# Kernel tuning notes

Hardware: AMD Instinct MI355X
Metric: run time of the kernel (lower is better)

Reference implementation:

```python
import jax, jax.numpy as jnp
import numpy as np

IN_F, HID, OUT_F, N_HEADS, BATCH = 256, 512, 2048, 8, 4096


def _kaiming_uniform(key, shape, fan_in):
    # kaiming_uniform_ with a=sqrt(5): gain = sqrt(2/(1+5)) = 1/sqrt(3)
    gain = 1.0 / np.sqrt(3.0)
    bound = gain * np.sqrt(3.0 / fan_in)  # = sqrt(1/fan_in)
    return jax.random.uniform(key, shape, jnp.float32, -bound, bound)


def setup_inputs() -> dict:
    key = jax.random.key(0)
    kx, ki, k1, k2, k3, k4 = jax.random.split(key, 6)
    X = jax.random.normal(kx, (BATCH, IN_F), jnp.float32)
    X_head_idx = jax.random.randint(ki, (BATCH,), 0, N_HEADS)
    # layer 1: in -> hidden
    W1 = _kaiming_uniform(k1, (N_HEADS, IN_F, HID), IN_F)
    b1 = jax.random.uniform(k2, (N_HEADS, HID), jnp.float32,
                            -1.0 / np.sqrt(IN_F), 1.0 / np.sqrt(IN_F))
    # layer 2: hidden -> out
    W2 = _kaiming_uniform(k3, (N_HEADS, HID, OUT_F), HID)
    b2 = jax.random.uniform(k4, (N_HEADS, OUT_F), jnp.float32,
                            -1.0 / np.sqrt(HID), 1.0 / np.sqrt(HID))
    return {"X": X, "X_head_idx": X_head_idx, "W1": W1, "b1": b1,
            "W2": W2, "b2": b2}


def _selective_linear(x, idx, W, b):
    # x: [B, in], W: [H, in, out], b: [H, out], idx: [B]
    # compute all heads densely, then select each sample's head
    y = jnp.einsum('bi,hio->bho', x, W) + b[None]   # [B, H, out]
    return jnp.take_along_axis(y, idx[:, None, None], axis=1)[:, 0, :]


def reference(X, X_head_idx, W1, b1, W2, b2):
    h = _selective_linear(X, X_head_idx, W1, b1)
    h = jax.nn.relu(h)
    out = _selective_linear(h, X_head_idx, W2, b2)
    return out
```

## Files before the change

### kernel.cpp

```cpp
#include <hip/hip_runtime.h>

#define IN_F 256
#define HID 512
#define OUT_F 2048
#define N_HEADS 8
#define BATCH 4096

typedef __bf16 bf16_t;
typedef bf16_t bf16x8 __attribute__((ext_vector_type(8)));
typedef float f32x4 __attribute__((ext_vector_type(4)));

typedef __attribute__((address_space(1))) const unsigned int gu32;
typedef __attribute__((address_space(3))) unsigned int lu32;

__device__ inline unsigned short f2bf(float f) {
  union { float f; unsigned u; } v; v.f = f;
  unsigned u = v.u;
  unsigned r = (u + 0x7FFFu + ((u >> 16) & 1u)) >> 16;
  return (unsigned short)r;
}

__global__ __launch_bounds__(1024) void bucket_kernel(const int* __restrict__ idx,
                                                      int* __restrict__ order,
                                                      int* __restrict__ offsets) {
  __shared__ int cnt[N_HEADS];
  __shared__ int base[N_HEADS + 1];
  __shared__ int cur[N_HEADS];
  int tid = threadIdx.x;
  if (tid < N_HEADS) cnt[tid] = 0;
  __syncthreads();
  for (int i = tid; i < BATCH; i += 1024) atomicAdd(&cnt[idx[i]], 1);
  __syncthreads();
  if (tid == 0) {
    int acc = 0;
    for (int h = 0; h < N_HEADS; ++h) { base[h] = acc; cur[h] = acc; acc += cnt[h]; }
    base[N_HEADS] = acc;
  }
  __syncthreads();
  if (tid < N_HEADS + 1) offsets[tid] = base[tid];
  for (int i = tid; i < BATCH; i += 1024) {
    int pos = atomicAdd(&cur[idx[i]], 1);
    order[pos] = i;
  }
}

__device__ inline void transpose64(const float* __restrict__ W,
                                   unsigned short* __restrict__ Wt,
                                   int K, int N, int b, int nt, int kt,
                                   float (*tile)[65]) {
  int per_head = nt * kt;
  int h = b / per_head;
  int rem = b % per_head;
  int n0 = (rem % nt) * 64;
  int k0 = (rem / nt) * 64;
  const float* Wh = W + (size_t)h * K * N;
  unsigned short* Wth = Wt + (size_t)h * K * N;
  int c = threadIdx.x & 63;
  int r0 = threadIdx.x >> 6;
  for (int rr = r0; rr < 64; rr += 4)
    tile[rr][c] = Wh[(size_t)(k0 + rr) * N + n0 + c];
  __syncthreads();
  for (int rr = r0; rr < 64; rr += 4)
    Wth[(size_t)(n0 + rr) * K + k0 + c] = f2bf(tile[c][rr]);
}

__global__ __launch_bounds__(256) void prep_kernel(const float* __restrict__ X,
                                                   const int* __restrict__ order,
                                                   unsigned short* __restrict__ Xg,
                                                   const float* __restrict__ W1,
                                                   unsigned short* __restrict__ W1t,
                                                   const float* __restrict__ W2,
                                                   unsigned short* __restrict__ W2t) {
  __shared__ float tile[64][65];
  int b = blockIdx.x;
  if (b < 512) {
    int c4 = threadIdx.x & 63;
    int rloc = threadIdx.x >> 6;
#pragma unroll
    for (int pass = 0; pass < 2; ++pass) {
      int p = b * 8 + pass * 4 + rloc;
      int src = order[p];
      float4 v = ((const float4*)(X + (size_t)src * IN_F))[c4];
      ushort4 o;
      o.x = f2bf(v.x); o.y = f2bf(v.y); o.z = f2bf(v.z); o.w = f2bf(v.w);
      ((ushort4*)(Xg + (size_t)p * IN_F))[c4] = o;
    }
  } else if (b < 768) {
    transpose64(W1, W1t, IN_F, HID, b - 512, HID / 64, IN_F / 64, tile);
  } else {
    transpose64(W2, W2t, HID, OUT_F, b - 768, OUT_F / 64, HID / 64, tile);
  }
}

template <int K, int NTOT, int EPI>
__global__ __launch_bounds__(256) void gemm128_kernel(const unsigned short* __restrict__ A,
                                                      const unsigned short* __restrict__ Wt,
                                                      const float* __restrict__ bias,
                                                      const int* __restrict__ offsets,
                                                      const int* __restrict__ order,
                                                      unsigned short* __restrict__ Hout,
                                                      float* __restrict__ Out) {
  constexpr int BM = 128, BN = 128, BK = 32;
  __shared__ __align__(16) unsigned short As[BM * BK];
  __shared__ __align__(16) unsigned short Bs[BN * BK];

  int my = blockIdx.y;
  int head = -1, row0 = 0, rows = 0, acc_t = 0;
#pragma unroll
  for (int h = 0; h < N_HEADS; ++h) {
    int o0 = offsets[h], o1 = offsets[h + 1];
    int cnt = o1 - o0;
    int t = (cnt + BM - 1) / BM;
    if (head < 0 && my < acc_t + t) {
      head = h;
      int lt = my - acc_t;
      row0 = o0 + lt * BM;
      rows = min(BM, cnt - lt * BM);
    }
    acc_t += t;
  }
  if (head < 0) return;

  int n0 = blockIdx.x * BN;
  const unsigned short* Bh = Wt + (size_t)head * (size_t)NTOT * K;

  int tid = threadIdx.x;
  int wave = tid >> 6;
  int lane = tid & 63;
  int q = lane >> 4;
  int l16 = lane & 15;

  int ldrow = lane >> 2;
  int ldcol = (lane & 3) * 8;
  int c0 = wave * 2, c1 = wave * 2 + 1;
  int ar0 = row0 + min(c0 * 16 + ldrow, rows - 1);
  int ar1 = row0 + min(c1 * 16 + ldrow, rows - 1);
  const unsigned short* aptr0 = A + (size_t)ar0 * K + ldcol;
  const unsigned short* aptr1 = A + (size_t)ar1 * K + ldcol;
  const unsigned short* bptr0 = Bh + (size_t)(n0 + c0 * 16 + ldrow) * K + ldcol;
  const unsigned short* bptr1 = Bh + (size_t)(n0 + c1 * 16 + ldrow) * K + ldcol;
  unsigned short* lA0 = As + c0 * 512;
  unsigned short* lA1 = As + c1 * 512;
  unsigned short* lB0 = Bs + c0 * 512;
  unsigned short* lB1 = Bs + c1 * 512;

  int w_m = wave >> 1, w_n = wave & 1;

  f32x4 acc[4][4];
#pragma unroll
  for (int i = 0; i < 4; ++i)
#pragma unroll
    for (int j = 0; j < 4; ++j) acc[i][j] = (f32x4){0.f, 0.f, 0.f, 0.f};

  for (int k0 = 0; k0 < K; k0 += BK) {
    __builtin_amdgcn_global_load_lds((gu32*)aptr0, (lu32*)lA0, 16, 0, 0);
    __builtin_amdgcn_global_load_lds((gu32*)aptr1, (lu32*)lA1, 16, 0, 0);
    __builtin_amdgcn_global_load_lds((gu32*)bptr0, (lu32*)lB0, 16, 0, 0);
    __builtin_amdgcn_global_load_lds((gu32*)bptr1, (lu32*)lB1, 16, 0, 0);
    aptr0 += BK; aptr1 += BK; bptr0 += BK; bptr1 += BK;
    __syncthreads();

    bf16x8 af[4], bfr[4];
#pragma unroll
    for (int i = 0; i < 4; ++i) {
      af[i] = *(const bf16x8*)(As + (w_m * 64 + i * 16 + l16) * BK + q * 8);
      bfr[i] = *(const bf16x8*)(Bs + (w_n * 64 + i * 16 + l16) * BK + q * 8);
    }
#pragma unroll
    for (int mi = 0; mi < 4; ++mi)
#pragma unroll
      for (int ni = 0; ni < 4; ++ni)
        acc[mi][ni] = __builtin_amdgcn_mfma_f32_16x16x32_bf16(af[mi], bfr[ni], acc[mi][ni], 0, 0, 0);
    __syncthreads();
  }

  float bval[4];
#pragma unroll
  for (int ni = 0; ni < 4; ++ni)
    bval[ni] = bias[(size_t)head * NTOT + n0 + w_n * 64 + ni * 16 + l16];

#pragma unroll
  for (int mi = 0; mi < 4; ++mi) {
#pragma unroll
    for (int r = 0; r < 4; ++r) {
      int m = w_m * 64 + mi * 16 + q * 4 + r;
      if (m < rows) {
        int p = row0 + m;
        if (EPI == 0) {
#pragma unroll
          for (int ni = 0; ni < 4; ++ni) {
            int n = n0 + w_n * 64 + ni * 16 + l16;
            float v = acc[mi][ni][r] + bval[ni];
            v = v > 0.f ? v : 0.f;
            Hout[(size_t)p * NTOT + n] = f2bf(v);
          }
        } else {
          int rg = order[p];
#pragma unroll
          for (int ni = 0; ni < 4; ++ni) {
            int n = n0 + w_n * 64 + ni * 16 + l16;
            Out[(size_t)rg * NTOT + n] = acc[mi][ni][r] + bval[ni];
          }
        }
      }
    }
  }
}

extern "C" void kernel_launch(void* const* d_in, const int* in_sizes, int n_in,
                              void* d_out, int out_size, void* d_ws, size_t ws_size,
                              hipStream_t stream) {
  const float* X = (const float*)d_in[0];
  const int* idxh = (const int*)d_in[1];
  const float* W1 = (const float*)d_in[2];
  const float* b1 = (const float*)d_in[3];
  const float* W2 = (const float*)d_in[4];
  const float* b2 = (const float*)d_in[5];
  float* out = (float*)d_out;

  char* ws = (char*)d_ws;
  int* order = (int*)ws;                     ws += (size_t)BATCH * 4;
  int* offsets = (int*)ws;                   ws += 64;
  unsigned short* Xg = (unsigned short*)ws;  ws += (size_t)BATCH * IN_F * 2;
  unsigned short* W1t = (unsigned short*)ws; ws += (size_t)N_HEADS * IN_F * HID * 2;
  unsigned short* W2t = (unsigned short*)ws; ws += (size_t)N_HEADS * HID * OUT_F * 2;
  unsigned short* Hb = (unsigned short*)ws;  ws += (size_t)BATCH * HID * 2;

  bucket_kernel<<<dim3(1), dim3(1024), 0, stream>>>(idxh, order, offsets);
  prep_kernel<<<dim3(2816), dim3(256), 0, stream>>>(X, order, Xg, W1, W1t, W2, W2t);

  constexpr int MT = BATCH / 128 + N_HEADS;
  gemm128_kernel<IN_F, HID, 0><<<dim3(HID / 128, MT), dim3(256), 0, stream>>>(
      Xg, W1t, b1, offsets, order, Hb, nullptr);
  gemm128_kernel<HID, OUT_F, 1><<<dim3(OUT_F / 128, MT), dim3(256), 0, stream>>>(
      Hb, W2t, b2, offsets, order, nullptr, out);
}
```

Before: 131.2 us.

## Fuse bucketing into prep, gather X inside GEMM1, widen BK with swizzled LDS

New measurement: 140.6 us. +7.2%, slower.

```diff
diff --git a/kernel.cpp b/kernel.cpp
--- a/kernel.cpp
+++ b/kernel.cpp
@@ -9,6 +9,7 @@
 typedef __bf16 bf16_t;
 typedef bf16_t bf16x8 __attribute__((ext_vector_type(8)));
 typedef float f32x4 __attribute__((ext_vector_type(4)));
+typedef unsigned short ushort8 __attribute__((ext_vector_type(8)));
 
 typedef __attribute__((address_space(1))) const unsigned int gu32;
 typedef __attribute__((address_space(3))) unsigned int lu32;
@@ -18,30 +19,6 @@
   unsigned u = v.u;
   unsigned r = (u + 0x7FFFu + ((u >> 16) & 1u)) >> 16;
   return (unsigned short)r;
-}
-
-__global__ __launch_bounds__(1024) void bucket_kernel(const int* __restrict__ idx,
-                                                      int* __restrict__ order,
-                                                      int* __restrict__ offsets) {
-  __shared__ int cnt[N_HEADS];
-  __shared__ int base[N_HEADS + 1];
-  __shared__ int cur[N_HEADS];
-  int tid = threadIdx.x;
-  if (tid < N_HEADS) cnt[tid] = 0;
-  __syncthreads();
-  for (int i = tid; i < BATCH; i += 1024) atomicAdd(&cnt[idx[i]], 1);
-  __syncthreads();
-  if (tid == 0) {
-    int acc = 0;
-    for (int h = 0; h < N_HEADS; ++h) { base[h] = acc; cur[h] = acc; acc += cnt[h]; }
-    base[N_HEADS] = acc;
-  }
-  __syncthreads();
-  if (tid < N_HEADS + 1) offsets[tid] = base[tid];
-  for (int i = tid; i < BATCH; i += 1024) {
-    int pos = atomicAdd(&cur[idx[i]], 1);
-    order[pos] = i;
-  }
 }
 
 __device__ inline void transpose64(const float* __restrict__ W,
@@ -64,43 +41,52 @@
     Wth[(size_t)(n0 + rr) * K + k0 + c] = f2bf(tile[c][rr]);
 }
 
-__global__ __launch_bounds__(256) void prep_kernel(const float* __restrict__ X,
-                                                   const int* __restrict__ order,
-                                                   unsigned short* __restrict__ Xg,
+__global__ __launch_bounds__(256) void prep_kernel(const int* __restrict__ idx,
+                                                   int* __restrict__ order,
+                                                   int* __restrict__ offsets,
                                                    const float* __restrict__ W1,
                                                    unsigned short* __restrict__ W1t,
                                                    const float* __restrict__ W2,
                                                    unsigned short* __restrict__ W2t) {
   __shared__ float tile[64][65];
+  __shared__ int cnt[N_HEADS];
+  __shared__ int base[N_HEADS + 1];
+  __shared__ int cur[N_HEADS];
   int b = blockIdx.x;
-  if (b < 512) {
-    int c4 = threadIdx.x & 63;
-    int rloc = threadIdx.x >> 6;
-#pragma unroll
-    for (int pass = 0; pass < 2; ++pass) {
-      int p = b * 8 + pass * 4 + rloc;
-      int src = order[p];
-      float4 v = ((const float4*)(X + (size_t)src * IN_F))[c4];
-      ushort4 o;
-      o.x = f2bf(v.x); o.y = f2bf(v.y); o.z = f2bf(v.z); o.w = f2bf(v.w);
-      ((ushort4*)(Xg + (size_t)p * IN_F))[c4] = o;
-    }
-  } else if (b < 768) {
-    transpose64(W1, W1t, IN_F, HID, b - 512, HID / 64, IN_F / 64, tile);
+  if (b == 0) {
+    int tid = threadIdx.x;
+    if (tid < N_HEADS) cnt[tid] = 0;
+    __syncthreads();
+    for (int i = tid; i < BATCH; i += 256) atomicAdd(&cnt[idx[i]], 1);
+    __syncthreads();
+    if (tid == 0) {
+      int acc = 0;
+      for (int h = 0; h < N_HEADS; ++h) { base[h] = acc; cur[h] = acc; acc += cnt[h]; }
+      base[N_HEADS] = acc;
+    }
+    __syncthreads();
+    if (tid < N_HEADS + 1) offsets[tid] = base[tid];
+    for (int i = tid; i < BATCH; i += 256) {
+      int pos = atomicAdd(&cur[idx[i]], 1);
+      order[pos] = i;
+    }
+  } else if (b < 257) {
+    transpose64(W1, W1t, IN_F, HID, b - 1, HID / 64, IN_F / 64, tile);
   } else {
-    transpose64(W2, W2t, HID, OUT_F, b - 768, OUT_F / 64, HID / 64, tile);
-  }
-}
-
-template <int K, int NTOT, int EPI>
-__global__ __launch_bounds__(256) void gemm128_kernel(const unsigned short* __restrict__ A,
-                                                      const unsigned short* __restrict__ Wt,
-                                                      const float* __restrict__ bias,
-                                                      const int* __restrict__ offsets,
-                                                      const int* __restrict__ order,
-                                                      unsigned short* __restrict__ Hout,
-                                                      float* __restrict__ Out) {
-  constexpr int BM = 128, BN = 128, BK = 32;
+    transpose64(W2, W2t, HID, OUT_F, b - 257, OUT_F / 64, HID / 64, tile);
+  }
+}
+
+template <int K, int NTOT, int EPI, int GATHER_A>
+__global__ __launch_bounds__(256) void gemm_kernel(const unsigned short* __restrict__ A,
+                                                   const float* __restrict__ Xf,
+                                                   const unsigned short* __restrict__ Wt,
+                                                   const float* __restrict__ bias,
+                                                   const int* __restrict__ offsets,
+                                                   const int* __restrict__ order,
+                                                   unsigned short* __restrict__ Hout,
+                                                   float* __restrict__ Out) {
+  constexpr int BM = 128, BN = 128, BK = 64;
   __shared__ __align__(16) unsigned short As[BM * BK];
   __shared__ __align__(16) unsigned short Bs[BN * BK];
 
@@ -129,23 +115,34 @@
   int lane = tid & 63;
   int q = lane >> 4;
   int l16 = lane & 15;
-
-  int ldrow = lane >> 2;
-  int ldcol = (lane & 3) * 8;
-  int c0 = wave * 2, c1 = wave * 2 + 1;
-  int ar0 = row0 + min(c0 * 16 + ldrow, rows - 1);
-  int ar1 = row0 + min(c1 * 16 + ldrow, rows - 1);
-  const unsigned short* aptr0 = A + (size_t)ar0 * K + ldcol;
-  const unsigned short* aptr1 = A + (size_t)ar1 * K + ldcol;
-  const unsigned short* bptr0 = Bh + (size_t)(n0 + c0 * 16 + ldrow) * K + ldcol;
-  const unsigned short* bptr1 = Bh + (size_t)(n0 + c1 * 16 + ldrow) * K + ldcol;
-  unsigned short* lA0 = As + c0 * 512;
-  unsigned short* lA1 = As + c1 * 512;
-  unsigned short* lB0 = Bs + c0 * 512;
-  unsigned short* lB1 = Bs + c1 * 512;
-
   int w_m = wave >> 1, w_n = wave & 1;
 
+  int srow = lane >> 3;
+  int seg = lane & 7;
+  int segl = seg ^ srow;
+
+  const unsigned short* bptr[4];
+#pragma unroll
+  for (int i = 0; i < 4; ++i) {
+    int rl = wave * 32 + i * 8 + srow;
+    bptr[i] = Bh + (size_t)(n0 + rl) * K + segl * 8;
+  }
+
+  const unsigned short* aptr[4];
+  const float* gptr[4];
+#pragma unroll
+  for (int i = 0; i < 4; ++i) {
+    int rl = wave * 32 + i * 8 + srow;
+    int pr = row0 + min(rl, rows - 1);
+    if (GATHER_A) {
+      gptr[i] = Xf + (size_t)order[pr] * K + segl * 8;
+      aptr[i] = nullptr;
+    } else {
+      aptr[i] = A + (size_t)pr * K + segl * 8;
+      gptr[i] = nullptr;
+    }
+  }
+
   f32x4 acc[4][4];
 #pragma unroll
   for (int i = 0; i < 4; ++i)
@@ -153,24 +150,49 @@
     for (int j = 0; j < 4; ++j) acc[i][j] = (f32x4){0.f, 0.f, 0.f, 0.f};
 
   for (int k0 = 0; k0 < K; k0 += BK) {
-    __builtin_amdgcn_global_load_lds((gu32*)aptr0, (lu32*)lA0, 16, 0, 0);
-    __builtin_amdgcn_global_load_lds((gu32*)aptr1, (lu32*)lA1, 16, 0, 0);
-    __builtin_amdgcn_global_load_lds((gu32*)bptr0, (lu32*)lB0, 16, 0, 0);
-    __builtin_amdgcn_global_load_lds((gu32*)bptr1, (lu32*)lB1, 16, 0, 0);
-    aptr0 += BK; aptr1 += BK; bptr0 += BK; bptr1 += BK;
-    __syncthreads();
-
-    bf16x8 af[4], bfr[4];
 #pragma unroll
     for (int i = 0; i < 4; ++i) {
-      af[i] = *(const bf16x8*)(As + (w_m * 64 + i * 16 + l16) * BK + q * 8);
-      bfr[i] = *(const bf16x8*)(Bs + (w_n * 64 + i * 16 + l16) * BK + q * 8);
-    }
-#pragma unroll
-    for (int mi = 0; mi < 4; ++mi)
-#pragma unroll
-      for (int ni = 0; ni < 4; ++ni)
-        acc[mi][ni] = __builtin_amdgcn_mfma_f32_16x16x32_bf16(af[mi], bfr[ni], acc[mi][ni], 0, 0, 0);
+      __builtin_amdgcn_global_load_lds((gu32*)bptr[i], (lu32*)(Bs + wave * 2048 + i * 512), 16, 0, 0);
+      bptr[i] += BK;
+    }
+    if (GATHER_A == 0) {
+#pragma unroll
+      for (int i = 0; i < 4; ++i) {
+        __builtin_amdgcn_global_load_lds((gu32*)aptr[i], (lu32*)(As + wave * 2048 + i * 512), 16, 0, 0);
+        aptr[i] += BK;
+      }
+    } else {
+#pragma unroll
+      for (int i = 0; i < 4; ++i) {
+        float4 v0 = *(const float4*)(gptr[i]);
+        float4 v1 = *(const float4*)(gptr[i] + 4);
+        gptr[i] += BK;
+        ushort8 o;
+        o[0] = f2bf(v0.x); o[1] = f2bf(v0.y); o[2] = f2bf(v0.z); o[3] = f2bf(v0.w);
+        o[4] = f2bf(v1.x); o[5] = f2bf(v1.y); o[6] = f2bf(v1.z); o[7] = f2bf(v1.w);
+        int rl = wave * 32 + i * 8 + srow;
+        *(ushort8*)(As + rl * 64 + seg * 8) = o;
+      }
+    }
+    __syncthreads();
+
+#pragma unroll
+    for (int kk = 0; kk < 2; ++kk) {
+      bf16x8 af[4], bfr[4];
+#pragma unroll
+      for (int i = 0; i < 4; ++i) {
+        int ra = w_m * 64 + i * 16 + l16;
+        int rb = w_n * 64 + i * 16 + l16;
+        int ps = ((kk * 4 + q) ^ (l16 & 7)) * 8;
+        af[i] = *(const bf16x8*)(As + ra * 64 + ps);
+        bfr[i] = *(const bf16x8*)(Bs + rb * 64 + ps);
+      }
+#pragma unroll
+      for (int mi = 0; mi < 4; ++mi)
+#pragma unroll
+        for (int ni = 0; ni < 4; ++ni)
+          acc[mi][ni] = __builtin_amdgcn_mfma_f32_16x16x32_bf16(af[mi], bfr[ni], acc[mi][ni], 0, 0, 0);
+    }
     __syncthreads();
   }
 
@@ -221,17 +243,15 @@
   char* ws = (char*)d_ws;
   int* order = (int*)ws;                     ws += (size_t)BATCH * 4;
   int* offsets = (int*)ws;                   ws += 64;
-  unsigned short* Xg = (unsigned short*)ws;  ws += (size_t)BATCH * IN_F * 2;
   unsigned short* W1t = (unsigned short*)ws; ws += (size_t)N_HEADS * IN_F * HID * 2;
   unsigned short* W2t = (unsigned short*)ws; ws += (size_t)N_HEADS * HID * OUT_F * 2;
   unsigned short* Hb = (unsigned short*)ws;  ws += (size_t)BATCH * HID * 2;
 
-  bucket_kernel<<<dim3(1), dim3(1024), 0, stream>>>(idxh, order, offsets);
-  prep_kernel<<<dim3(2816), dim3(256), 0, stream>>>(X, order, Xg, W1, W1t, W2, W2t);
+  prep_kernel<<<dim3(2305), dim3(256), 0, stream>>>(idxh, order, offsets, W1, W1t, W2, W2t);
 
   constexpr int MT = BATCH / 128 + N_HEADS;
-  gemm128_kernel<IN_F, HID, 0><<<dim3(HID / 128, MT), dim3(256), 0, stream>>>(
-      Xg, W1t, b1, offsets, order, Hb, nullptr);
-  gemm128_kernel<HID, OUT_F, 1><<<dim3(OUT_F / 128, MT), dim3(256), 0, stream>>>(
-      Hb, W2t, b2, offsets, order, nullptr, out);
-}
+  gemm_kernel<IN_F, HID, 0, 1><<<dim3(HID / 128, MT), dim3(256), 0, stream>>>(
+      nullptr, X, W1t, b1, offsets, order, Hb, nullptr);
+  gemm_kernel<HID, OUT_F, 1, 0><<<dim3(OUT_F / 128, MT), dim3(256), 0, stream>>>(
+      Hb, nullptr, W2t, b2, offsets, order, nullptr, out);
+}
```
